# Kernel optimization log

Measured on AMD Instinct MI355X. Metric: run time of the kernel, lower is better.

The kernel has to match this reference:

```python
import jax, jax.numpy as jnp
import numpy as np
from jax import lax

NUM_HEADS = 8
EPS = 1e-12  # F.normalize default eps


def _l2norm(t):
    # F.normalize(t, dim=-1): t / max(||t||_2, eps)
    n = jnp.sqrt(jnp.sum(t * t, axis=-1, keepdims=True))
    return t / jnp.maximum(n, EPS)


def setup_inputs() -> dict:
    key = jax.random.key(0)
    k1, k2, k3, k4 = jax.random.split(key, 4)
    b, c, h, w = 16, 384, 64, 64
    x = jax.random.normal(k1, (b, c, h, w), dtype=jnp.float32)
    # 1x1 conv weights stored as (out, in); depthwise 3x3 as (3c, 1, 3, 3)
    w_qkv = jax.random.normal(k2, (3 * c, c), dtype=jnp.float32) * (1.0 / np.sqrt(c))
    w_dw = jax.random.normal(k3, (3 * c, 1, 3, 3), dtype=jnp.float32) * (1.0 / 3.0)
    w_proj = jax.random.normal(k4, (c, c), dtype=jnp.float32) * (1.0 / np.sqrt(c))
    temperature = jnp.ones((1, NUM_HEADS, 1, 1), dtype=jnp.float32)
    return {"x": x, "w_qkv": w_qkv, "w_dw": w_dw, "w_proj": w_proj,
            "temperature": temperature}


def reference(x, w_qkv, w_dw, w_proj, temperature):
    b, c, h, w = x.shape
    hw = h * w
    d = c // NUM_HEADS  # per-head channel dim

    # 1x1 pointwise conv: (b,c,h,w) x (3c,c) -> (b,3c,h,w)
    qkv = jnp.einsum('bchw,oc->bohw', x, w_qkv)
    # depthwise 3x3 conv, groups = 3c, padding SAME, no bias
    qkv = lax.conv_general_dilated(
        qkv, w_dw, window_strides=(1, 1), padding='SAME',
        feature_group_count=3 * c,
        dimension_numbers=('NCHW', 'OIHW', 'NCHW'))

    q, k, v = jnp.split(qkv, 3, axis=1)
    q = q.reshape(b, NUM_HEADS, d, hw)
    k = k.reshape(b, NUM_HEADS, d, hw)
    v = v.reshape(b, NUM_HEADS, d, hw)

    q = _l2norm(q)
    k = _l2norm(k)

    # transposed (channel) attention: scores over channel dim, (b,H,d,d)
    scores = jnp.einsum('bhdn,bhen->bhde', q, k) * temperature
    attn = jax.nn.softmax(scores, axis=-1)

    out = jnp.einsum('bhde,bhen->bhdn', attn, v).reshape(b, c, h, w)
    out = jnp.einsum('bchw,oc->bohw', out, w_proj)
    return out
```

## Files before the change

### kernel.cpp

```cpp
#include <hip/hip_runtime.h>
#include <hip/hip_bf16.h>
#include <math.h>

#define B_   16
#define C_   384
#define C3_  1152
#define HW_  4096
#define NH_  8
#define D_   48

typedef _Float16 f16x8 __attribute__((ext_vector_type(8)));
typedef _Float16 f16x4 __attribute__((ext_vector_type(4)));
typedef _Float16 f16x2 __attribute__((ext_vector_type(2)));
typedef float    f32x4 __attribute__((ext_vector_type(4)));

#define ASM_VMCNT(n) asm volatile("s_waitcnt vmcnt(" #n ")" ::: "memory")

__global__ __launch_bounds__(256) void conv_w_all(
    const float* __restrict__ wqkv, const float* __restrict__ wproj,
    _Float16* __restrict__ oq, _Float16* __restrict__ op)
{
    const int nq = C3_ * C_ / 4;
    const int np = C_ * C_ / 4;
    int i = blockIdx.x * 256 + threadIdx.x;
    const float* src; _Float16* dst; int j;
    if (i < nq) { src = wqkv; dst = oq; j = i; }
    else if (i < nq + np) { src = wproj; dst = op; j = i - nq; }
    else return;
    float4 v = *(const float4*)&src[(size_t)j * 4];
    f16x4 h = { (_Float16)v.x, (_Float16)v.y, (_Float16)v.z, (_Float16)v.w };
    *(f16x4*)&dst[(size_t)j * 4] = h;
}

__global__ __launch_bounds__(256) void transpose_to_f16(
    const float* __restrict__ x, _Float16* __restrict__ xt)
{
    const int b  = blockIdx.z;
    const int k0 = blockIdx.y * 64;
    const int n0 = blockIdx.x * 64;
    __shared__ float sm[64][65];
    const float* xb = x + (size_t)b * C_ * HW_;
    _Float16* xtb = xt + (size_t)b * HW_ * C_;
    const int t = threadIdx.x;
    #pragma unroll
    for (int i = 0; i < 4; ++i) {
        int row = (t >> 4) + i * 16;
        int col = (t & 15) * 4;
        float4 v = *(const float4*)&xb[(size_t)(k0 + row) * HW_ + n0 + col];
        sm[row][col] = v.x; sm[row][col+1] = v.y; sm[row][col+2] = v.z; sm[row][col+3] = v.w;
    }
    __syncthreads();
    #pragma unroll
    for (int i = 0; i < 2; ++i) {
        int nl = (t >> 3) + i * 32;
        int ks = (t & 7) * 8;
        f16x8 h;
        #pragma unroll
        for (int j = 0; j < 8; ++j) h[j] = (_Float16)sm[ks + j][nl];
        *(f16x8*)&xtb[(size_t)(n0 + nl) * C_ + k0 + ks] = h;
    }
}

template<int M, bool F32OUT>
__global__ __launch_bounds__(256, 2) void mfma_gemm(
    const _Float16* __restrict__ Wb,
    const _Float16* __restrict__ XT,
    void* __restrict__ Cv, long long xstride, long long cstride)
{
    constexpr int K = 384;
    constexpr int BK = 32;
    constexpr int NSTEP = K / BK;
    constexpr int MB = M / 128;
    __shared__ _Float16 Ash[3][128 * BK];
    __shared__ _Float16 Bsh[3][256 * BK];

    const int nwg = MB * 16 * B_;
    const int cpx = nwg >> 3;
    const int bid = blockIdx.x;
    const int L   = (bid & 7) * cpx + (bid >> 3);
    const int m0  = (L % MB) * 128;
    const int nb  = L / MB;
    const int n0  = (nb & 15) * 256;
    const int b   = nb >> 4;

    const _Float16* __restrict__ XTb = XT + (size_t)b * xstride;
    const int t = threadIdx.x;
    const int l = t & 63, w = t >> 6;
    const int frow = l & 15, kseg16 = l >> 4;

    auto stage = [&](int d, int kt) {
        const int kk = kt * BK;
        #pragma unroll
        for (int i = 0; i < 2; ++i) {
            const int u = i * 256 + t;
            const int row = u >> 2, slot = u & 3;
            const int scol = slot ^ (row & 3) ^ ((row >> 2) & 1);
            const _Float16* ga = Wb + (size_t)(m0 + row) * K + kk + scol * 8;
            __builtin_amdgcn_global_load_lds(
                (const __attribute__((address_space(1))) void*)ga,
                (__attribute__((address_space(3))) void*)((char*)&Ash[d][0] + u * 16),
                16, 0, 0);
        }
        #pragma unroll
        for (int i = 0; i < 4; ++i) {
            const int u = i * 256 + t;
            const int row = u >> 2, slot = u & 3;
            const int scol = slot ^ (row & 3) ^ ((row >> 2) & 1);
            const _Float16* gb = XTb + (size_t)(n0 + row) * K + kk + scol * 8;
            __builtin_amdgcn_global_load_lds(
                (const __attribute__((address_space(1))) void*)gb,
                (__attribute__((address_space(3))) void*)((char*)&Bsh[d][0] + u * 16),
                16, 0, 0);
        }
    };

    f32x4 acc[8][4] = {};

    stage(0, 0);
    stage(1, 1);
    #pragma unroll
    for (int kt = 0; kt < NSTEP; ++kt) {
        const int cur = kt % 3;
        if (kt + 1 < NSTEP) { ASM_VMCNT(6); } else { ASM_VMCNT(0); }
        __builtin_amdgcn_sched_barrier(0);
        __builtin_amdgcn_s_barrier();
        __builtin_amdgcn_sched_barrier(0);
        if (kt + 2 < NSTEP) stage((kt + 2) % 3, kt + 2);
        f16x8 af[8], bfr[4];
        #pragma unroll
        for (int mi = 0; mi < 8; ++mi) {
            const int rA = mi * 16 + frow;
            const int cs = kseg16 ^ (rA & 3) ^ ((rA >> 2) & 1);
            af[mi] = *(const f16x8*)&Ash[cur][rA * BK + cs * 8];
        }
        #pragma unroll
        for (int ni = 0; ni < 4; ++ni) {
            const int rB = w * 64 + ni * 16 + frow;
            const int cs = kseg16 ^ (rB & 3) ^ ((rB >> 2) & 1);
            bfr[ni] = *(const f16x8*)&Bsh[cur][rB * BK + cs * 8];
        }
        __builtin_amdgcn_s_setprio(1);
        #pragma unroll
        for (int mi = 0; mi < 8; ++mi)
            #pragma unroll
            for (int ni = 0; ni < 4; ++ni)
                acc[mi][ni] = __builtin_amdgcn_mfma_f32_16x16x32_f16(
                    bfr[ni], af[mi], acc[mi][ni], 0, 0, 0);
        __builtin_amdgcn_s_setprio(0);
    }
    const int pxl = (l >> 4) * 4;
    const int chl = l & 15;
    if constexpr (F32OUT) {
        float* Co = (float*)Cv + (size_t)b * cstride;
        #pragma unroll
        for (int mi = 0; mi < 8; ++mi)
            #pragma unroll
            for (int ni = 0; ni < 4; ++ni)
                *(f32x4*)&Co[(size_t)(m0 + mi * 16 + chl) * HW_
                             + n0 + w * 64 + ni * 16 + pxl] = acc[mi][ni];
    } else {
        _Float16* Co = (_Float16*)Cv + (size_t)b * cstride;
        #pragma unroll
        for (int mi = 0; mi < 8; ++mi)
            #pragma unroll
            for (int ni = 0; ni < 4; ++ni) {
                f16x4 h;
                #pragma unroll
                for (int r = 0; r < 4; ++r) h[r] = (_Float16)acc[mi][ni][r];
                *(f16x4*)&Co[(size_t)(m0 + mi * 16 + chl) * HW_
                             + n0 + w * 64 + ni * 16 + pxl] = h;
            }
    }
}

__global__ __launch_bounds__(256) void dwconv_norm(
    _Float16* __restrict__ buf, const float* __restrict__ wdw,
    float* __restrict__ nqinv, float* __restrict__ nkinv)
{
    const int plane = blockIdx.x;
    const int ch = plane % C3_, b = plane / C3_;
    __shared__ _Float16 smh[64 * 72];
    __shared__ float wsum[4];
    _Float16* g = buf + (size_t)plane * HW_;
    const int t = threadIdx.x;
    #pragma unroll
    for (int i = 0; i < 2; ++i) {
        const int u = i * 256 + t;
        f16x8 v = *(const f16x8*)&g[u * 8];
        *(f16x8*)&smh[(u >> 3) * 72 + (u & 7) * 8] = v;
    }
    float w[9];
    #pragma unroll
    for (int j = 0; j < 9; ++j) w[j] = wdw[ch * 9 + j];
    __syncthreads();
    float ssq = 0.f;
    #pragma unroll
    for (int i = 0; i < 2; ++i) {
        const int u = i * 256 + t;
        const int y = u >> 3, c0 = (u & 7) * 8;
        float r[3][10];
        #pragma unroll
        for (int dy = 0; dy < 3; ++dy) {
            const int yy = y + dy - 1;
            if (yy < 0 || yy > 63) {
                #pragma unroll
                for (int j = 0; j < 10; ++j) r[dy][j] = 0.f;
            } else {
                f16x8 v = *(const f16x8*)&smh[yy * 72 + c0];
                #pragma unroll
                for (int j = 0; j < 8; ++j) r[dy][j + 1] = (float)v[j];
                r[dy][0] = (c0 > 0)  ? (float)smh[yy * 72 + c0 - 1] : 0.f;
                r[dy][9] = (c0 < 56) ? (float)smh[yy * 72 + c0 + 8] : 0.f;
            }
        }
        f16x8 o;
        #pragma unroll
        for (int j = 0; j < 8; ++j) {
            float s = 0.f;
            #pragma unroll
            for (int dy = 0; dy < 3; ++dy)
                #pragma unroll
                for (int dx = 0; dx < 3; ++dx)
                    s = fmaf(w[dy * 3 + dx], r[dy][j + dx], s);
            o[j] = (_Float16)s;
            ssq = fmaf(s, s, ssq);
        }
        *(f16x8*)&g[u * 8] = o;
    }
    if (ch < 2 * C_) {
        #pragma unroll
        for (int m = 1; m < 64; m <<= 1) ssq += __shfl_xor(ssq, m);
        if ((t & 63) == 0) wsum[t >> 6] = ssq;
        __syncthreads();
        if (t == 0) {
            float tot = wsum[0] + wsum[1] + wsum[2] + wsum[3];
            float inv = 1.f / fmaxf(sqrtf(tot), 1e-12f);
            (ch < C_ ? nqinv : nkinv)[b * C_ + (ch % C_)] = inv;
        }
    }
}

__global__ __launch_bounds__(256) void scores_mfma(
    const _Float16* __restrict__ buf, float* __restrict__ sp)
{
    const int bh = blockIdx.x;
    const int ks = blockIdx.y;
    const int b = bh >> 3, h = bh & 7;
    const _Float16* qbase = buf + ((size_t)b * C3_ + (size_t)h * D_) * HW_;
    const _Float16* kbase = qbase + (size_t)C_ * HW_;
    const int t = threadIdx.x, l = t & 63, w = t >> 6;
    const int frow = l & 15, kseg = (l >> 4) * 8;
    const int p0 = ks * 1024 + w * 256;

    f32x4 acc[3][3] = {};
    #pragma unroll 2
    for (int st = 0; st < 8; ++st) {
        const int p = p0 + st * 32 + kseg;
        f16x8 qf[3], kf[3];
        #pragma unroll
        for (int mi = 0; mi < 3; ++mi)
            qf[mi] = *(const f16x8*)&qbase[(size_t)(mi * 16 + frow) * HW_ + p];
        #pragma unroll
        for (int ni = 0; ni < 3; ++ni)
            kf[ni] = *(const f16x8*)&kbase[(size_t)(ni * 16 + frow) * HW_ + p];
        #pragma unroll
        for (int mi = 0; mi < 3; ++mi)
            #pragma unroll
            for (int ni = 0; ni < 3; ++ni)
                acc[mi][ni] = __builtin_amdgcn_mfma_f32_16x16x32_f16(
                    qf[mi], kf[ni], acc[mi][ni], 0, 0, 0);
    }
    __shared__ float red[4][D_ * D_];
    #pragma unroll
    for (int mi = 0; mi < 3; ++mi)
        #pragma unroll
        for (int ni = 0; ni < 3; ++ni)
            #pragma unroll
            for (int r = 0; r < 4; ++r)
                red[w][(mi * 16 + (l >> 4) * 4 + r) * D_ + ni * 16 + (l & 15)] =
                    acc[mi][ni][r];
    __syncthreads();
    float* out = sp + ((size_t)ks * 128 + bh) * (D_ * D_);
    const float* rf = &red[0][0];
    for (int i = t; i < D_ * D_; i += 256)
        out[i] = rf[i] + rf[2304 + i] + rf[4608 + i] + rf[6912 + i];
}

__global__ __launch_bounds__(256) void softmax_k(
    const float* __restrict__ sp, const float* __restrict__ nqinv,
    const float* __restrict__ nkinv, const float* __restrict__ temp,
    float* __restrict__ attn)
{
    const int row = blockIdx.x * 4 + (threadIdx.x >> 6);
    const int bh = row / D_, d = row % D_;
    const int h = bh & 7;
    const int e = threadIdx.x & 63;
    float s = -INFINITY;
    if (e < D_) {
        float raw = 0.f;
        #pragma unroll
        for (int ks = 0; ks < 4; ++ks)
            raw += sp[((size_t)ks * 128 + bh) * (D_ * D_) + d * D_ + e];
        s = raw * nqinv[bh * D_ + d] * nkinv[bh * D_ + e] * temp[h];
    }
    float m = s;
    #pragma unroll
    for (int off = 1; off < 64; off <<= 1) m = fmaxf(m, __shfl_xor(m, off));
    float p = (e < D_) ? expf(s - m) : 0.f;
    float sum = p;
    #pragma unroll
    for (int off = 1; off < 64; off <<= 1) sum += __shfl_xor(sum, off);
    if (e < D_) attn[(size_t)bh * (D_ * D_) + d * D_ + e] = p / sum;
}

__global__ __launch_bounds__(256) void pv_kernel(
    _Float16* __restrict__ buf, const float* __restrict__ attn)
{
    const int b = blockIdx.z, h = blockIdx.y;
    const int p0 = blockIdx.x * 512 + threadIdx.x * 2;
    __shared__ float a4[48][48];
    const float* ab = attn + ((size_t)b * 8 + h) * (D_ * D_);
    for (int i = threadIdx.x; i < D_ * D_; i += 256) ((float*)a4)[i] = ab[i];
    __syncthreads();
    const _Float16* vbase = buf + ((size_t)b * C3_ + 2 * C_ + (size_t)h * D_) * HW_;
    float2 acc[48];
    #pragma unroll
    for (int d = 0; d < 48; ++d) { acc[d].x = 0.f; acc[d].y = 0.f; }
    #pragma unroll 1
    for (int e4 = 0; e4 < 12; ++e4) {
        float2 vv[4];
        #pragma unroll
        for (int j = 0; j < 4; ++j) {
            f16x2 h2 = *(const f16x2*)&vbase[(size_t)(e4 * 4 + j) * HW_ + p0];
            vv[j].x = (float)h2[0]; vv[j].y = (float)h2[1];
        }
        #pragma unroll
        for (int d = 0; d < 48; ++d) {
            float4 a = *(const float4*)&a4[d][e4 * 4];
            acc[d].x = fmaf(a.x, vv[0].x, fmaf(a.y, vv[1].x, fmaf(a.z, vv[2].x, fmaf(a.w, vv[3].x, acc[d].x))));
            acc[d].y = fmaf(a.x, vv[0].y, fmaf(a.y, vv[1].y, fmaf(a.z, vv[2].y, fmaf(a.w, vv[3].y, acc[d].y))));
        }
    }
    _Float16* xt2b = buf + (size_t)b * C3_ * HW_;
    #pragma unroll
    for (int px = 0; px < 2; ++px) {
        f16x8 tmp[6];
        #pragma unroll
        for (int d = 0; d < 48; ++d) tmp[d >> 3][d & 7] = (_Float16)(px ? acc[d].y : acc[d].x);
        f16x8* dst = (f16x8*)&xt2b[(size_t)(p0 + px) * C_ + h * D_];
        #pragma unroll
        for (int j = 0; j < 6; ++j) dst[j] = tmp[j];
    }
}

extern "C" void kernel_launch(void* const* d_in, const int* in_sizes, int n_in,
                              void* d_out, int out_size, void* d_ws, size_t ws_size,
                              hipStream_t stream)
{
    const float* x      = (const float*)d_in[0];
    const float* w_qkv  = (const float*)d_in[1];
    const float* w_dw   = (const float*)d_in[2];
    const float* w_proj = (const float*)d_in[3];
    const float* temp   = (const float*)d_in[4];
    float* out = (float*)d_out;

    _Float16* buf = (_Float16*)d_ws;
    float* nqinv = (float*)(buf + (size_t)B_ * C3_ * HW_);
    float* nkinv = nqinv + 6144;
    float* sp    = nkinv + 6144;
    float* attn  = sp + (size_t)4 * 128 * D_ * D_;
    _Float16* wqkv_h  = (_Float16*)(attn + (size_t)128 * D_ * D_);
    _Float16* wproj_h = wqkv_h + (size_t)C3_ * C_;
    _Float16* xt1     = wproj_h + (size_t)C_ * C_;

    conv_w_all<<<(C3_ * C_ / 4 + C_ * C_ / 4 + 255) / 256, 256, 0, stream>>>(
        w_qkv, w_proj, wqkv_h, wproj_h);
    transpose_to_f16<<<dim3(64, 6, 16), 256, 0, stream>>>(x, xt1);

    mfma_gemm<C3_, false><<<dim3(9 * 16 * 16), 256, 0, stream>>>(
        wqkv_h, xt1, buf, (long long)HW_ * C_, (long long)C3_ * HW_);

    dwconv_norm<<<B_ * C3_, 256, 0, stream>>>(buf, w_dw, nqinv, nkinv);

    scores_mfma<<<dim3(128, 4), 256, 0, stream>>>(buf, sp);

    softmax_k<<<1536, 256, 0, stream>>>(sp, nqinv, nkinv, temp, attn);

    pv_kernel<<<dim3(8, 8, 16), 256, 0, stream>>>(buf, attn);

    mfma_gemm<C_, true><<<dim3(3 * 16 * 16), 256, 0, stream>>>(
        wproj_h, buf, out, (long long)C3_ * HW_, (long long)C_ * HW_);
}
```

Baseline: 299.1 us.

## Pre-pack QKV GEMM operands into MFMA fragment layout and load directly to registers

The weight and input transpose kernels now write f16 data already arranged as per-lane MFMA fragments (512-element units). The QKV GEMM is replaced by a kernel that loads those fragments straight from global memory into registers with double buffering, with no LDS staging and no barriers. The aim is to remove LDS traffic and synchronisation from the main projection GEMM. The cost is that operand reuse now relies on the caches instead of shared memory, and the loads may be less latency-tolerant. The weight conversion is split into two launches.

Result: slower. 334.9 us (+12.0%).

```diff
diff --git a/kernel.cpp b/kernel.cpp
--- a/kernel.cpp
+++ b/kernel.cpp
@@ -16,31 +16,41 @@
 
 #define ASM_VMCNT(n) asm volatile("s_waitcnt vmcnt(" #n ")" ::: "memory")
 
-__global__ __launch_bounds__(256) void conv_w_all(
-    const float* __restrict__ wqkv, const float* __restrict__ wproj,
-    _Float16* __restrict__ oq, _Float16* __restrict__ op)
-{
-    const int nq = C3_ * C_ / 4;
-    const int np = C_ * C_ / 4;
+__global__ __launch_bounds__(256) void conv_w_plain(
+    const float* __restrict__ w, _Float16* __restrict__ wh, int n4)
+{
     int i = blockIdx.x * 256 + threadIdx.x;
-    const float* src; _Float16* dst; int j;
-    if (i < nq) { src = wqkv; dst = oq; j = i; }
-    else if (i < nq + np) { src = wproj; dst = op; j = i - nq; }
-    else return;
-    float4 v = *(const float4*)&src[(size_t)j * 4];
-    f16x4 h = { (_Float16)v.x, (_Float16)v.y, (_Float16)v.z, (_Float16)v.w };
-    *(f16x4*)&dst[(size_t)j * 4] = h;
-}
-
-__global__ __launch_bounds__(256) void transpose_to_f16(
-    const float* __restrict__ x, _Float16* __restrict__ xt)
+    if (i < n4) {
+        float4 v = *(const float4*)&w[(size_t)i * 4];
+        f16x4 h = { (_Float16)v.x, (_Float16)v.y, (_Float16)v.z, (_Float16)v.w };
+        *(f16x4*)&wh[(size_t)i * 4] = h;
+    }
+}
+
+__global__ __launch_bounds__(256) void conv_w_frag(
+    const float* __restrict__ w, _Float16* __restrict__ wf)
+{
+    const int u = blockIdx.x * 4 + (threadIdx.x >> 6);
+    const int l = threadIdx.x & 63;
+    if (u >= (C3_ / 16) * 12) return;
+    const int mf = u / 12, ks = u % 12;
+    const int row = mf * 16 + (l & 15);
+    const int col = ks * 32 + (l >> 4) * 8;
+    float4 v0 = *(const float4*)&w[(size_t)row * C_ + col];
+    float4 v1 = *(const float4*)&w[(size_t)row * C_ + col + 4];
+    f16x8 h = { (_Float16)v0.x, (_Float16)v0.y, (_Float16)v0.z, (_Float16)v0.w,
+                (_Float16)v1.x, (_Float16)v1.y, (_Float16)v1.z, (_Float16)v1.w };
+    *(f16x8*)&wf[(size_t)u * 512 + l * 8] = h;
+}
+
+__global__ __launch_bounds__(256) void transpose_to_frag(
+    const float* __restrict__ x, _Float16* __restrict__ xtf)
 {
     const int b  = blockIdx.z;
     const int k0 = blockIdx.y * 64;
     const int n0 = blockIdx.x * 64;
     __shared__ float sm[64][65];
     const float* xb = x + (size_t)b * C_ * HW_;
-    _Float16* xtb = xt + (size_t)b * HW_ * C_;
     const int t = threadIdx.x;
     #pragma unroll
     for (int i = 0; i < 4; ++i) {
@@ -50,15 +60,82 @@
         sm[row][col] = v.x; sm[row][col+1] = v.y; sm[row][col+2] = v.z; sm[row][col+3] = v.w;
     }
     __syncthreads();
-    #pragma unroll
-    for (int i = 0; i < 2; ++i) {
-        int nl = (t >> 3) + i * 32;
-        int ks = (t & 7) * 8;
+    const int w = t >> 6, l = t & 63;
+    const int pxl = w * 16 + (l & 15);
+    const int ck  = (l >> 4) * 8;
+    #pragma unroll
+    for (int ksl = 0; ksl < 2; ++ksl) {
         f16x8 h;
         #pragma unroll
-        for (int j = 0; j < 8; ++j) h[j] = (_Float16)sm[ks + j][nl];
-        *(f16x8*)&xtb[(size_t)(n0 + nl) * C_ + k0 + ks] = h;
-    }
+        for (int j = 0; j < 8; ++j) h[j] = (_Float16)sm[ksl * 32 + ck + j][pxl];
+        const size_t unit = ((size_t)(b * 256 + (n0 >> 4) + w) * 12 + (k0 >> 5) + ksl);
+        *(f16x8*)&xtf[unit * 512 + l * 8] = h;
+    }
+}
+
+__global__ __launch_bounds__(256, 2) void mfma_gemm_frag(
+    const _Float16* __restrict__ Wf,
+    const _Float16* __restrict__ XTf,
+    _Float16* __restrict__ Co)
+{
+    constexpr int MB = C3_ / 128;
+    const int nwg = MB * 16 * B_;
+    const int cpx = nwg >> 3;
+    const int bid = blockIdx.x;
+    const int L   = (bid & 7) * cpx + (bid >> 3);
+    const int m0  = (L % MB) * 128;
+    const int nb  = L / MB;
+    const int nt  = nb & 15;
+    const int b   = nb >> 4;
+
+    const int t = threadIdx.x;
+    const int l = t & 63, w = t >> 6;
+
+    const _Float16* Abase = Wf  + (size_t)(m0 >> 4) * 12 * 512 + l * 8;
+    const _Float16* Bbase = XTf + ((size_t)(b * 256 + nt * 16 + w * 4)) * 12 * 512 + l * 8;
+
+    f32x4 acc[8][4] = {};
+    f16x8 aA[8], bA[4], aB[8], bB[4];
+
+    #pragma unroll
+    for (int mi = 0; mi < 8; ++mi) aA[mi] = *(const f16x8*)(Abase + (size_t)mi * 12 * 512);
+    #pragma unroll
+    for (int ni = 0; ni < 4; ++ni) bA[ni] = *(const f16x8*)(Bbase + (size_t)ni * 12 * 512);
+
+    #pragma unroll
+    for (int ks = 0; ks < 12; ++ks) {
+        f16x8* ac = (ks & 1) ? aB : aA;
+        f16x8* bc = (ks & 1) ? bB : bA;
+        f16x8* an = (ks & 1) ? aA : aB;
+        f16x8* bn = (ks & 1) ? bA : bB;
+        if (ks + 1 < 12) {
+            #pragma unroll
+            for (int mi = 0; mi < 8; ++mi)
+                an[mi] = *(const f16x8*)(Abase + (size_t)mi * 12 * 512 + (ks + 1) * 512);
+            #pragma unroll
+            for (int ni = 0; ni < 4; ++ni)
+                bn[ni] = *(const f16x8*)(Bbase + (size_t)ni * 12 * 512 + (ks + 1) * 512);
+        }
+        #pragma unroll
+        for (int mi = 0; mi < 8; ++mi)
+            #pragma unroll
+            for (int ni = 0; ni < 4; ++ni)
+                acc[mi][ni] = __builtin_amdgcn_mfma_f32_16x16x32_f16(
+                    bc[ni], ac[mi], acc[mi][ni], 0, 0, 0);
+    }
+    const int pxl = (l >> 4) * 4;
+    const int chl = l & 15;
+    _Float16* Cb = Co + (size_t)b * C3_ * HW_;
+    #pragma unroll
+    for (int mi = 0; mi < 8; ++mi)
+        #pragma unroll
+        for (int ni = 0; ni < 4; ++ni) {
+            f16x4 h;
+            #pragma unroll
+            for (int r = 0; r < 4; ++r) h[r] = (_Float16)acc[mi][ni][r];
+            *(f16x4*)&Cb[(size_t)(m0 + mi * 16 + chl) * HW_
+                         + nt * 256 + w * 64 + ni * 16 + pxl] = h;
+        }
 }
 
 template<int M, bool F32OUT>
@@ -116,8 +193,7 @@
 
     f32x4 acc[8][4] = {};
 
-    stage(0, 0);
-    stage(1, 1);
+    stage(0, 0); stage(1, 1);
     #pragma unroll
     for (int kt = 0; kt < NSTEP; ++kt) {
         const int cur = kt % 3;
@@ -369,16 +445,15 @@
     float* nkinv = nqinv + 6144;
     float* sp    = nkinv + 6144;
     float* attn  = sp + (size_t)4 * 128 * D_ * D_;
-    _Float16* wqkv_h  = (_Float16*)(attn + (size_t)128 * D_ * D_);
-    _Float16* wproj_h = wqkv_h + (size_t)C3_ * C_;
-    _Float16* xt1     = wproj_h + (size_t)C_ * C_;
-
-    conv_w_all<<<(C3_ * C_ / 4 + C_ * C_ / 4 + 255) / 256, 256, 0, stream>>>(
-        w_qkv, w_proj, wqkv_h, wproj_h);
-    transpose_to_f16<<<dim3(64, 6, 16), 256, 0, stream>>>(x, xt1);
-
-    mfma_gemm<C3_, false><<<dim3(9 * 16 * 16), 256, 0, stream>>>(
-        wqkv_h, xt1, buf, (long long)HW_ * C_, (long long)C3_ * HW_);
+    _Float16* wqkv_f  = (_Float16*)(attn + (size_t)128 * D_ * D_);
+    _Float16* wproj_h = wqkv_f + (size_t)C3_ * C_;
+    _Float16* xtf     = wproj_h + (size_t)C_ * C_;
+
+    conv_w_frag<<<(C3_ / 16) * 12 / 4, 256, 0, stream>>>(w_qkv, wqkv_f);
+    conv_w_plain<<<(C_ * C_ / 4 + 255) / 256, 256, 0, stream>>>(w_proj, wproj_h, C_ * C_ / 4);
+    transpose_to_frag<<<dim3(64, 6, 16), 256, 0, stream>>>(x, xtf);
+
+    mfma_gemm_frag<<<dim3(9 * 16 * 16), 256, 0, stream>>>(wqkv_f, xtf, buf);
 
     dwconv_norm<<<B_ * C3_, 256, 0, stream>>>(buf, w_dw, nqinv, nkinv);
 
```
